# Optimization experiments

Hardware: AMD Instinct MI355X
Metric: run time of the kernel (lower is better)

Reference implementation:

```python
import jax, jax.numpy as jnp
import numpy as np

TEMP = 1.0  # softmax temperature (init kwarg)


def setup_inputs() -> dict:
    key = jax.random.key(0)
    k1, k2 = jax.random.split(key)
    two_n, d_model = 512, 256
    embeddings = jax.random.normal(k1, (two_n, d_model), dtype=jnp.float32)
    targets = jax.random.uniform(k2, (two_n, 1), dtype=jnp.float32)
    return {"embeddings": embeddings, "targets": targets}


def reference(embeddings, targets):
    # embeddings: [2N, d_model], targets: [2N, 1]
    two_n = embeddings.shape[0]
    # label distance d[i,j] = |t_i - t_j|
    d = jnp.abs(targets - targets.T)                                  # [2N, 2N]
    # exp similarity s[i,j] = exp(-||e_i - e_j||_2 / temp)
    diff = embeddings[:, None, :] - embeddings[None, :, :]            # [2N, 2N, d]
    s = jnp.exp(-jnp.linalg.norm(diff, axis=-1) / TEMP)               # [2N, 2N]
    off_diag = 1.0 - jnp.eye(two_n, dtype=s.dtype)                    # [2N, 2N]
    # mask3[i,k,j] = (d[i,j] >= d[i,k]) * (j != i)
    mask3 = (d[:, None, :] >= d[:, :, None]).astype(s.dtype) * off_diag[:, None, :]
    # denominator D[i,k] = sum_j mask3[i,k,j] * s[i,j]
    denom = jnp.einsum('ikj,ij->ik', mask3, s)                        # [2N, 2N]
    loss = jnp.log(s / denom) * off_diag
    return -jnp.sum(loss) / (two_n * (two_n - 1))
```

## Files before the change

### kernel.cpp

```cpp
#include <hip/hip_runtime.h>
#include <math.h>

#define TWO_N 512
#define DM    256
#define NT    256

#define OFF_TS   1048576
#define OFF_INV  1050624
#define OFF_BSUM 1052672

#define ACC4(acc, A, B) { float _d;                      \
    _d = (A).x - (B).x; acc += _d * _d;                  \
    _d = (A).y - (B).y; acc += _d * _d;                  \
    _d = (A).z - (B).z; acc += _d * _d;                  \
    _d = (A).w - (B).w; acc += _d * _d; }

__global__ __launch_bounds__(NT) void supcr_dist_sort(
    const float* __restrict__ E, const float* __restrict__ T,
    float* __restrict__ Rp, float* __restrict__ ts_g, int* __restrict__ inv_g)
{
    const int bid = blockIdx.x;
    const int t   = threadIdx.x;

    __shared__ float tv[TWO_N];
    tv[t]       = T[t];
    tv[t + 256] = T[t + 256];
    __syncthreads();

    if (bid < 256) {
        __shared__ float4 As4[32 * 65];
        __shared__ float4 Bs4[32 * 65];
        __shared__ int    cnt[32 * 9];
        __shared__ int    invc_s[32];

        const int it = bid >> 4, jt = bid & 15;

        {
            const int cl = t >> 3;
            const int ss = t & 7;
            const int c  = jt * 32 + cl;
            const float tc = tv[c];
            int n = 0;
            const int j0 = ss * 64;
            #pragma unroll 8
            for (int j = j0; j < j0 + 64; ++j) {
                const float tj = tv[j];
                n += (tj < tc) || (tj == tc && j < c);
            }
            cnt[cl * 9 + ss] = n;
        }

        const float4* __restrict__ E4 = reinterpret_cast<const float4*>(E);
        for (int idx = t; idx < 32 * 64; idx += NT) {
            const int row = idx >> 6, c4 = idx & 63;
            As4[row * 65 + c4] = E4[(it * 32 + row) * 64 + c4];
            Bs4[row * 65 + c4] = E4[(jt * 32 + row) * 64 + c4];
        }
        __syncthreads();

        if (t < 32) {
            int r = 0;
            #pragma unroll
            for (int ss = 0; ss < 8; ++ss) r += cnt[t * 9 + ss];
            invc_s[t] = r;
        }
        __syncthreads();

        const int ty = t >> 4, tx = t & 15;
        float a00 = 0.f, a01 = 0.f, a10 = 0.f, a11 = 0.f;
        #pragma unroll 8
        for (int k4 = 0; k4 < 64; ++k4) {
            const float4 a0 = As4[ty * 65 + k4];
            const float4 a1 = As4[(ty + 16) * 65 + k4];
            const float4 b0 = Bs4[tx * 65 + k4];
            const float4 b1 = Bs4[(tx + 16) * 65 + k4];
            ACC4(a00, a0, b0); ACC4(a01, a0, b1);
            ACC4(a10, a1, b0); ACC4(a11, a1, b1);
        }
        const int r0 = it * 32 + ty, r1 = r0 + 16;
        const int m0 = invc_s[tx],  m1 = invc_s[tx + 16];
        Rp[r0 * TWO_N + m0] = sqrtf(a00);
        Rp[r0 * TWO_N + m1] = sqrtf(a01);
        Rp[r1 * TWO_N + m0] = sqrtf(a10);
        Rp[r1 * TWO_N + m1] = sqrtf(a11);
    } else {
        #pragma unroll
        for (int w = 0; w < 2; ++w) {
            const int c  = t + w * 256;
            const float tc = tv[c];
            int r = 0;
            #pragma unroll 8
            for (int j = 0; j < TWO_N; ++j) {
                const float tj = tv[j];
                r += (tj < tc) || (tj == tc && j < c);
            }
            ts_g[r]  = tc;
            inv_g[c] = r;
        }
    }
}

__global__ __launch_bounds__(NT) void supcr_rows(
    const float* __restrict__ T, const float* __restrict__ Rp,
    const float* __restrict__ ts_g, const int* __restrict__ inv_g,
    double* __restrict__ bsums)
{
    const int i = blockIdx.x;
    const int t = threadIdx.x;

    __shared__ float  ts[TWO_N];
    __shared__ float  rv[TWO_N];
    __shared__ float  P[TWO_N];
    __shared__ double red[NT];

    const int   mi = inv_g[i];
    const float ti = T[i];
    const float* __restrict__ row = Rp + (size_t)i * TWO_N;

    #pragma unroll
    for (int w = 0; w < 2; ++w) {
        const int m = t + w * 256;
        ts[m] = ts_g[m];
        const float r = row[m];
        rv[m] = r;
        P[m]  = (m == mi) ? 0.f : __expf(-r);
    }
    __syncthreads();

    for (int off = 1; off < TWO_N; off <<= 1) {
        const float v0 = (t >= off)       ? P[t - off]       : 0.f;
        const float v1 = (t + 256 >= off) ? P[t + 256 - off] : 0.f;
        __syncthreads();
        P[t]       += v0;
        P[t + 256] += v1;
        __syncthreads();
    }

    const float Stot = P[TWO_N - 1];

    float local = 0.f;
    #pragma unroll
    for (int w = 0; w < 2; ++w) {
        const int m = t + w * 256;
        if (m == mi) continue;
        const float theta = fabsf(ti - ts[m]);

        const int nl = mi + 1;
        int pos = 0;
        #pragma unroll
        for (int step = 512; step >= 1; step >>= 1) {
            const int np = pos + step;
            if (np <= nl && fabsf(ti - ts[np - 1]) >= theta) pos = np;
        }
        const int cl = nl - pos;

        const int nr = TWO_N - mi;
        int pr = 0;
        #pragma unroll
        for (int step = 512; step >= 1; step >>= 1) {
            const int np = pr + step;
            if (np <= nr && fabsf(ti - ts[mi + np - 1]) < theta) pr = np;
        }

        const int L  = mi - cl + 1;
        const int Rr = mi + pr - 1;
        float inner = 0.f;
        if (Rr >= L) inner = P[Rr] - ((L > 0) ? P[L - 1] : 0.f);
        const float denom = Stot - inner;
        local += -rv[m] - logf(denom);
    }

    red[t] = (double)local;
    __syncthreads();
    for (int off = NT / 2; off > 0; off >>= 1) {
        if (t < off) red[t] += red[t + off];
        __syncthreads();
    }
    if (t == 0) bsums[i] = red[0];
}

__global__ __launch_bounds__(TWO_N) void supcr_finalize(
    const double* __restrict__ bsums, float* __restrict__ out)
{
    __shared__ double red[TWO_N];
    const int t = threadIdx.x;
    red[t] = bsums[t];
    __syncthreads();
    for (int off = TWO_N / 2; off > 0; off >>= 1) {
        if (t < off) red[t] += red[t + off];
        __syncthreads();
    }
    if (t == 0)
        out[0] = (float)(-red[0] / (double)((long long)TWO_N * (TWO_N - 1)));
}

extern "C" void kernel_launch(void* const* d_in, const int* in_sizes, int n_in,
                              void* d_out, int out_size, void* d_ws, size_t ws_size,
                              hipStream_t stream) {
    (void)in_sizes; (void)n_in; (void)out_size; (void)ws_size;
    const float* E = (const float*)d_in[0];
    const float* T = (const float*)d_in[1];
    float* out = (float*)d_out;

    char* ws = (char*)d_ws;
    float*  Rp    = (float*)(ws);
    float*  ts_g  = (float*)(ws + OFF_TS);
    int*    inv_g = (int*)(ws + OFF_INV);
    double* bsums = (double*)(ws + OFF_BSUM);

    supcr_dist_sort<<<257, NT, 0, stream>>>(E, T, Rp, ts_g, inv_g);
    supcr_rows<<<TWO_N, NT, 0, stream>>>(T, Rp, ts_g, inv_g, bsums);
    supcr_finalize<<<1, TWO_N, 0, stream>>>(bsums, out);
}
```

Baseline: 89.23 us.

## Fuse distance, rank sort and row loss into one per-row kernel

Merges the distance/sort kernel and the per-row loss kernel into a single kernel, so each block computes its row's distances directly using wave-level shuffle reductions. Each block also recomputes the target ranks itself rather than reading them from global memory. This removes one kernel launch and the round trip of the 1 MB distance matrix through global memory. In exchange the O(N^2) rank computation is repeated in every block, and the distance work moves from a shared-memory tiled scheme to per-row global loads with shuffle reductions.

```diff
diff --git a/kernel.cpp b/kernel.cpp
--- a/kernel.cpp
+++ b/kernel.cpp
@@ -5,125 +5,86 @@
 #define DM    256
 #define NT    256
 
-#define OFF_TS   1048576
-#define OFF_INV  1050624
-#define OFF_BSUM 1052672
-
-#define ACC4(acc, A, B) { float _d;                      \
-    _d = (A).x - (B).x; acc += _d * _d;                  \
-    _d = (A).y - (B).y; acc += _d * _d;                  \
-    _d = (A).z - (B).z; acc += _d * _d;                  \
-    _d = (A).w - (B).w; acc += _d * _d; }
-
-__global__ __launch_bounds__(NT) void supcr_dist_sort(
+__global__ __launch_bounds__(NT) void supcr_fused(
     const float* __restrict__ E, const float* __restrict__ T,
-    float* __restrict__ Rp, float* __restrict__ ts_g, int* __restrict__ inv_g)
-{
-    const int bid = blockIdx.x;
-    const int t   = threadIdx.x;
-
-    __shared__ float tv[TWO_N];
-    tv[t]       = T[t];
-    tv[t + 256] = T[t + 256];
-    __syncthreads();
-
-    if (bid < 256) {
-        __shared__ float4 As4[32 * 65];
-        __shared__ float4 Bs4[32 * 65];
-        __shared__ int    cnt[32 * 9];
-        __shared__ int    invc_s[32];
-
-        const int it = bid >> 4, jt = bid & 15;
-
-        {
-            const int cl = t >> 3;
-            const int ss = t & 7;
-            const int c  = jt * 32 + cl;
-            const float tc = tv[c];
-            int n = 0;
-            const int j0 = ss * 64;
-            #pragma unroll 8
-            for (int j = j0; j < j0 + 64; ++j) {
-                const float tj = tv[j];
-                n += (tj < tc) || (tj == tc && j < c);
-            }
-            cnt[cl * 9 + ss] = n;
-        }
-
-        const float4* __restrict__ E4 = reinterpret_cast<const float4*>(E);
-        for (int idx = t; idx < 32 * 64; idx += NT) {
-            const int row = idx >> 6, c4 = idx & 63;
-            As4[row * 65 + c4] = E4[(it * 32 + row) * 64 + c4];
-            Bs4[row * 65 + c4] = E4[(jt * 32 + row) * 64 + c4];
-        }
-        __syncthreads();
-
-        if (t < 32) {
-            int r = 0;
-            #pragma unroll
-            for (int ss = 0; ss < 8; ++ss) r += cnt[t * 9 + ss];
-            invc_s[t] = r;
-        }
-        __syncthreads();
-
-        const int ty = t >> 4, tx = t & 15;
-        float a00 = 0.f, a01 = 0.f, a10 = 0.f, a11 = 0.f;
-        #pragma unroll 8
-        for (int k4 = 0; k4 < 64; ++k4) {
-            const float4 a0 = As4[ty * 65 + k4];
-            const float4 a1 = As4[(ty + 16) * 65 + k4];
-            const float4 b0 = Bs4[tx * 65 + k4];
-            const float4 b1 = Bs4[(tx + 16) * 65 + k4];
-            ACC4(a00, a0, b0); ACC4(a01, a0, b1);
-            ACC4(a10, a1, b0); ACC4(a11, a1, b1);
-        }
-        const int r0 = it * 32 + ty, r1 = r0 + 16;
-        const int m0 = invc_s[tx],  m1 = invc_s[tx + 16];
-        Rp[r0 * TWO_N + m0] = sqrtf(a00);
-        Rp[r0 * TWO_N + m1] = sqrtf(a01);
-        Rp[r1 * TWO_N + m0] = sqrtf(a10);
-        Rp[r1 * TWO_N + m1] = sqrtf(a11);
-    } else {
-        #pragma unroll
-        for (int w = 0; w < 2; ++w) {
-            const int c  = t + w * 256;
-            const float tc = tv[c];
-            int r = 0;
-            #pragma unroll 8
-            for (int j = 0; j < TWO_N; ++j) {
-                const float tj = tv[j];
-                r += (tj < tc) || (tj == tc && j < c);
-            }
-            ts_g[r]  = tc;
-            inv_g[c] = r;
-        }
-    }
-}
-
-__global__ __launch_bounds__(NT) void supcr_rows(
-    const float* __restrict__ T, const float* __restrict__ Rp,
-    const float* __restrict__ ts_g, const int* __restrict__ inv_g,
     double* __restrict__ bsums)
 {
-    const int i = blockIdx.x;
-    const int t = threadIdx.x;
+    const int i    = blockIdx.x;
+    const int t    = threadIdx.x;
+    const int lane = t & 63;
+    const int wv   = t >> 6;
 
+    __shared__ float  tv[TWO_N];
     __shared__ float  ts[TWO_N];
+    __shared__ int    inv_s[TWO_N];
     __shared__ float  rv[TWO_N];
     __shared__ float  P[TWO_N];
     __shared__ double red[NT];
+    __shared__ int    mi_s;
 
-    const int   mi = inv_g[i];
-    const float ti = T[i];
-    const float* __restrict__ row = Rp + (size_t)i * TWO_N;
+    tv[t]       = T[t];
+    tv[t + 256] = T[t + 256];
+
+    const float4* __restrict__ E4 = reinterpret_cast<const float4*>(E);
+    const float4 ei4 = E4[i * 64 + lane];
+
+    __syncthreads();
+
+    const float ti = tv[i];
 
     #pragma unroll
     for (int w = 0; w < 2; ++w) {
-        const int m = t + w * 256;
-        ts[m] = ts_g[m];
-        const float r = row[m];
-        rv[m] = r;
-        P[m]  = (m == mi) ? 0.f : __expf(-r);
+        const int c  = t + w * 256;
+        const float tc = tv[c];
+        int r = 0;
+        #pragma unroll 8
+        for (int j = 0; j < TWO_N; ++j) {
+            const float tj = tv[j];
+            r += (tj < tc) || (tj == tc && j < c);
+        }
+        ts[r]    = tc;
+        inv_s[c] = r;
+        if (c == i) mi_s = r;
+    }
+    __syncthreads();
+
+    for (int jj = 0; jj < 128; jj += 4) {
+        const int j0 = (wv << 7) + jj;
+        const float4 b0 = E4[((j0 + 0) << 6) + lane];
+        const float4 b1 = E4[((j0 + 1) << 6) + lane];
+        const float4 b2 = E4[((j0 + 2) << 6) + lane];
+        const float4 b3 = E4[((j0 + 3) << 6) + lane];
+        float v0, v1, v2, v3;
+        {
+            float dx, dy, dz, dw;
+            dx = ei4.x - b0.x; dy = ei4.y - b0.y; dz = ei4.z - b0.z; dw = ei4.w - b0.w;
+            v0 = dx * dx + dy * dy + dz * dz + dw * dw;
+            dx = ei4.x - b1.x; dy = ei4.y - b1.y; dz = ei4.z - b1.z; dw = ei4.w - b1.w;
+            v1 = dx * dx + dy * dy + dz * dz + dw * dw;
+            dx = ei4.x - b2.x; dy = ei4.y - b2.y; dz = ei4.z - b2.z; dw = ei4.w - b2.w;
+            v2 = dx * dx + dy * dy + dz * dz + dw * dw;
+            dx = ei4.x - b3.x; dy = ei4.y - b3.y; dz = ei4.z - b3.z; dw = ei4.w - b3.w;
+            v3 = dx * dx + dy * dy + dz * dz + dw * dw;
+        }
+        #pragma unroll
+        for (int m = 1; m < 64; m <<= 1) {
+            v0 += __shfl_xor(v0, m, 64);
+            v1 += __shfl_xor(v1, m, 64);
+            v2 += __shfl_xor(v2, m, 64);
+            v3 += __shfl_xor(v3, m, 64);
+        }
+        if (lane == 0) {
+            const float r0 = sqrtf(v0), r1 = sqrtf(v1);
+            const float r2 = sqrtf(v2), r3 = sqrtf(v3);
+            rv[j0 + 0] = r0;
+            rv[j0 + 1] = r1;
+            rv[j0 + 2] = r2;
+            rv[j0 + 3] = r3;
+            P[inv_s[j0 + 0]] = (j0 + 0 == i) ? 0.f : __expf(-r0);
+            P[inv_s[j0 + 1]] = (j0 + 1 == i) ? 0.f : __expf(-r1);
+            P[inv_s[j0 + 2]] = (j0 + 2 == i) ? 0.f : __expf(-r2);
+            P[inv_s[j0 + 3]] = (j0 + 3 == i) ? 0.f : __expf(-r3);
+        }
     }
     __syncthreads();
 
@@ -137,13 +98,14 @@
     }
 
     const float Stot = P[TWO_N - 1];
+    const int   mi   = mi_s;
 
     float local = 0.f;
     #pragma unroll
     for (int w = 0; w < 2; ++w) {
-        const int m = t + w * 256;
-        if (m == mi) continue;
-        const float theta = fabsf(ti - ts[m]);
+        const int k = t + w * 256;
+        if (k == i) continue;
+        const float theta = fabsf(ti - tv[k]);
 
         const int nl = mi + 1;
         int pos = 0;
@@ -167,7 +129,7 @@
         float inner = 0.f;
         if (Rr >= L) inner = P[Rr] - ((L > 0) ? P[L - 1] : 0.f);
         const float denom = Stot - inner;
-        local += -rv[m] - logf(denom);
+        local += -rv[k] - logf(denom);
     }
 
     red[t] = (double)local;
@@ -201,14 +163,8 @@
     const float* E = (const float*)d_in[0];
     const float* T = (const float*)d_in[1];
     float* out = (float*)d_out;
+    double* bsums = (double*)d_ws;
 
-    char* ws = (char*)d_ws;
-    float*  Rp    = (float*)(ws);
-    float*  ts_g  = (float*)(ws + OFF_TS);
-    int*    inv_g = (int*)(ws + OFF_INV);
-    double* bsums = (double*)(ws + OFF_BSUM);
-
-    supcr_dist_sort<<<257, NT, 0, stream>>>(E, T, Rp, ts_g, inv_g);
-    supcr_rows<<<TWO_N, NT, 0, stream>>>(T, Rp, ts_g, inv_g, bsums);
+    supcr_fused<<<TWO_N, NT, 0, stream>>>(E, T, bsums);
     supcr_finalize<<<1, TWO_N, 0, stream>>>(bsums, out);
 }
```

After: 117.0 us. +31.1%, slower.
